# Performance work log

Measured on AMD Instinct MI355X. Metric: run time of the kernel, lower is better.

The kernel has to match this reference:

```python
import jax, jax.numpy as jnp
import numpy as np

# Physics config (DPhysConfig defaults for the tracked robot)
MASS = 40.0        # robot mass [kg]
GRAV = 9.8         # gravity magnitude
STIFF = 1000.0     # terrain stiffness
DAMP = 100.0       # terrain damping
OMEGA_MAX = 2.0    # angular velocity clamp
DT = 0.01          # integration step [s]
LY = 0.6           # robot width (track separation)
RES = 0.1          # grid resolution [m/cell]


def skew(v):
    # v: (..., 3) -> (..., 3, 3)
    z = jnp.zeros_like(v[..., 0])
    return jnp.stack([
        jnp.stack([z, -v[..., 2], v[..., 1]], -1),
        jnp.stack([v[..., 2], z, -v[..., 0]], -1),
        jnp.stack([-v[..., 1], v[..., 0], z], -1)], -2)


def normalized(x, eps=1e-6):
    return x / jnp.clip(jnp.linalg.norm(x, axis=-1, keepdims=True), eps)


def bilinear(grid, xq, yq):
    # grid: (B, H, W) over [-H*RES/2, H*RES/2] x [-W*RES/2, W*RES/2]; xq, yq: (B, N)
    B, H, W = grid.shape
    u = jnp.clip((xq + H * RES / 2) / RES, 0.0, H - 1.001)
    v = jnp.clip((yq + W * RES / 2) / RES, 0.0, W - 1.001)
    u0 = jnp.floor(u).astype(jnp.int32)
    v0 = jnp.floor(v).astype(jnp.int32)
    du, dv = u - u0, v - v0
    b = jnp.arange(B)[:, None]
    g00 = grid[b, u0, v0]
    g10 = grid[b, u0 + 1, v0]
    g01 = grid[b, u0, v0 + 1]
    g11 = grid[b, u0 + 1, v0 + 1]
    return (g00 * (1 - du) * (1 - dv) + g10 * du * (1 - dv)
            + g01 * (1 - du) * dv + g11 * du * dv)


def inertia_inv(points, mass):
    # points: (N, 3) body-frame point masses -> inverse inertia (3, 3)
    mp = mass / points.shape[0]
    x, y, z = points[:, 0], points[:, 1], points[:, 2]
    Ixx = (mp * (y ** 2 + z ** 2)).sum()
    Iyy = (mp * (x ** 2 + z ** 2)).sum()
    Izz = (mp * (x ** 2 + y ** 2)).sum()
    Ixy = -(mp * x * y).sum()
    Ixz = -(mp * x * z).sum()
    Iyz = -(mp * y * z).sum()
    I = jnp.stack([jnp.stack([Ixx, Ixy, Ixz]),
                   jnp.stack([Ixy, Iyy, Iyz]),
                   jnp.stack([Ixz, Iyz, Izz])])
    return jnp.linalg.inv(I)


def _forward(z_grid, friction, controls, robot_points, x0, xd0, R0, omega0):
    dtype = z_grid.dtype
    I_inv = inertia_inv(robot_points, MASS)          # (3,3), joints fixed -> constant
    gx = jnp.gradient(z_grid, axis=1) / RES          # dz/dx on grid
    gy = jnp.gradient(z_grid, axis=2) / RES          # dz/dy on grid
    maskL = (robot_points[:, 1] < 0).astype(dtype)   # (N,) left track points
    maskR = 1.0 - maskL                              # right track points
    F_grav = MASS * GRAV * jnp.array([0.0, 0.0, -1.0], dtype=dtype)
    clamp = MASS * GRAV

    def dynamics(state, ctrl):
        x, xd, R, omega = state
        # world-frame body points: x_points @ R^T + x
        pts = jnp.einsum('nj,bkj->bnk', robot_points, R) + x[:, None]      # (B,N,3)
        xd_pts = xd[:, None] + jnp.cross(omega[:, None, :], pts - x[:, None], axis=-1)
        px, py = pts[..., 0], pts[..., 1]
        z = bilinear(z_grid, px, py)[..., None]                            # (B,N,1)
        nrm = normalized(jnp.stack([-bilinear(gx, px, py),
                                    -bilinear(gy, px, py),
                                    jnp.ones_like(px)], -1))               # (B,N,3)
        fr = bilinear(friction, px, py)[..., None]                         # (B,N,1)
        dh = pts[..., 2:3] - z
        in_c = jax.nn.sigmoid(-10.0 * dh)
        xd_n = jnp.sum(xd_pts * nrm, -1, keepdims=True)
        F_r = -(STIFF * dh + DAMP * xd_n) * nrm
        F_r = jnp.clip(F_r * in_c / jnp.sum(in_c, 1, keepdims=True), -clamp, clamp)
        thrust = normalized(R[..., 0])                                     # (B,3) first column
        Nmag = jnp.linalg.norm(F_r, axis=2)                                # (B,N)
        v, w = ctrl[:, 0], ctrl[:, 1]
        vL = (v - w * LY / 2)[:, None, None]
        vR = (v + w * LY / 2)[:, None, None]
        cmd = (maskL[None, :, None] * vL + maskR[None, :, None] * vR) * thrust[:, None, :]
        slip = fr * (cmd - xd_pts)
        slip_tau = slip - jnp.sum(slip * nrm, -1, keepdims=True) * nrm
        F_f = jnp.clip(Nmag[..., None] * slip_tau, -clamp, clamp)
        torque = jnp.sum(jnp.cross(pts - x[:, None], F_r + F_f, axis=-1), axis=1)
        omega_d = jnp.clip(torque @ I_inv.T, -OMEGA_MAX, OMEGA_MAX)
        xdd = (F_grav[None] + F_r.sum(1) + F_f.sum(1)) / MASS
        return xdd, omega_d

    def rot_step(R, omega, eps=1e-6):
        # Rodrigues' formula
        Ox = skew(omega)
        th = jnp.linalg.norm(omega, axis=-1)[:, None, None]
        Oxn = Ox / jnp.clip(th, eps)
        I3 = jnp.eye(3, dtype=R.dtype)
        return R @ (I3 + Oxn * jnp.sin(th * DT) + (Oxn @ Oxn) * (1 - jnp.cos(th * DT)))

    def step(state, ctrl):
        x, xd, R, omega = state
        xdd, omega_d = dynamics(state, ctrl)
        xd = xd + xdd * DT          # semi-implicit Euler, as in update_state
        x = x + xd * DT
        omega = omega + omega_d * DT
        R = rot_step(R, omega)
        return (x, xd, R, omega), x

    _, Xs = jax.lax.scan(step, (x0, xd0, R0, omega0), jnp.swapaxes(controls, 0, 1))
    return jnp.swapaxes(Xs, 0, 1)   # (B, T, 3) trajectory positions


def setup_inputs() -> dict:
    key = jax.random.key(0)
    ks = jax.random.split(key, 5)
    B, T, N, H, W = 64, 500, 128, 256, 256
    z_grid = jax.random.uniform(ks[0], (B, H, W), dtype=jnp.float32) * 0.2
    friction = jax.random.uniform(ks[1], (B, H, W), dtype=jnp.float32)
    controls = jax.random.normal(ks[2], (B, T, 2), dtype=jnp.float32) * jnp.array([1.0, 0.5], jnp.float32)
    robot_points = (jax.random.uniform(ks[3], (N, 3), dtype=jnp.float32) - 0.5) \
        * jnp.array([1.0, 0.6, 0.2], jnp.float32)
    x0 = jax.random.normal(ks[4], (B, 3), dtype=jnp.float32) * 0.1 + jnp.array([0.0, 0.0, 0.3], jnp.float32)
    xd0 = jnp.zeros((B, 3), jnp.float32)
    R0 = jnp.tile(jnp.eye(3, dtype=jnp.float32), (B, 1, 1))
    omega0 = jnp.zeros((B, 3), jnp.float32)
    return {"z_grid": z_grid, "friction": friction, "controls": controls,
            "robot_points": robot_points, "x0": x0, "xd0": xd0, "R0": R0, "omega0": omega0}


def reference(z_grid, friction, controls, robot_points, x0, xd0, R0, omega0):
    return _forward(z_grid, friction, controls, robot_points, x0, xd0, R0, omega0)
```

## Files before the change

kernel.cpp:

```cpp
#include <hip/hip_runtime.h>
#include <math.h>

#define GH 256
#define GW 256

typedef float f4 __attribute__((ext_vector_type(4), aligned(4)));
typedef float f2 __attribute__((ext_vector_type(2), aligned(4)));
typedef float f4l __attribute__((ext_vector_type(4)));

template<int CTRL, int RMASK>
__device__ __forceinline__ float dpp_add(float v) {
    int r = __builtin_amdgcn_update_dpp(0, __builtin_bit_cast(int, v), CTRL, RMASK, 0xF, true);
    return v + __builtin_bit_cast(float, r);
}
template<int CTRL, int RMASK>
__device__ __forceinline__ float dpp_max(float v) {
    int r = __builtin_amdgcn_update_dpp(0, __builtin_bit_cast(int, v), CTRL, RMASK, 0xF, true);
    return fmaxf(v, __builtin_bit_cast(float, r));
}

__device__ __forceinline__ float wave_sum63(float v) {
    v = dpp_add<0xB1, 0xF>(v);
    v = dpp_add<0x4E, 0xF>(v);
    v = dpp_add<0x141, 0xF>(v);
    v = dpp_add<0x140, 0xF>(v);
    v = dpp_add<0x142, 0xA>(v);
    v = dpp_add<0x143, 0xC>(v);
    return v;
}
__device__ __forceinline__ float wave_max63(float v) {
    v = dpp_max<0xB1, 0xF>(v);
    v = dpp_max<0x4E, 0xF>(v);
    v = dpp_max<0x141, 0xF>(v);
    v = dpp_max<0x140, 0xF>(v);
    v = dpp_max<0x142, 0xA>(v);
    v = dpp_max<0x143, 0xC>(v);
    return v;
}
__device__ __forceinline__ float rl63(float v) {
    return __builtin_bit_cast(float, __builtin_amdgcn_readlane(__builtin_bit_cast(int, v), 63));
}

__device__ __forceinline__ float frcp(float x)  { return __builtin_amdgcn_rcpf(x); }
__device__ __forceinline__ float frsq(float x)  { return __builtin_amdgcn_rsqf(x); }
__device__ __forceinline__ float fexp2(float x) { return __builtin_amdgcn_exp2f(x); }

__global__ __launch_bounds__(128) void dphys_kernel(
    const float* __restrict__ z_grid,
    const float* __restrict__ friction,
    const float* __restrict__ controls,
    const float* __restrict__ robot_points,
    const float* __restrict__ x0,
    const float* __restrict__ xd0,
    const float* __restrict__ R0,
    const float* __restrict__ omega0,
    float* __restrict__ out,
    int T)
{
    const int b = blockIdx.x;
    const int tid = threadIdx.x;
    const int wv = tid >> 6;
    __shared__ f4l ldsX[2][2][2];
    __shared__ f4l ldsY[2][2];

    const float* __restrict__ zg = z_grid + (size_t)b * (GH * GW);
    const float* __restrict__ fg = friction + (size_t)b * (GH * GW);
    const float* __restrict__ ct = controls + (size_t)b * (T * 2);
    float* __restrict__ ob = out + (size_t)b * (T * 3);

    const float ppx = robot_points[tid * 3 + 0];
    const float ppy = robot_points[tid * 3 + 1];
    const float ppz = robot_points[tid * 3 + 2];
    const bool isL = (ppy < 0.0f);

    float I6[6];
    I6[0] = ppy * ppy + ppz * ppz;
    I6[1] = ppx * ppx + ppz * ppz;
    I6[2] = ppx * ppx + ppy * ppy;
    I6[3] = ppx * ppy;
    I6[4] = ppx * ppz;
    I6[5] = ppy * ppz;
    #pragma unroll
    for (int k = 0; k < 6; ++k) I6[k] = rl63(wave_sum63(I6[k]));
    if ((tid & 63) == 63) {
        f4l t0; t0.x = I6[0]; t0.y = I6[1]; t0.z = I6[2]; t0.w = I6[3];
        f4l t1; t1.x = I6[4]; t1.y = I6[5]; t1.z = 0.f; t1.w = 0.f;
        ldsY[wv][0] = t0; ldsY[wv][1] = t1;
    }
    __syncthreads();
    {
        f4l o0 = ldsY[wv ^ 1][0], o1 = ldsY[wv ^ 1][1];
        I6[0] += o0.x; I6[1] += o0.y; I6[2] += o0.z;
        I6[3] += o0.w; I6[4] += o1.x; I6[5] += o1.y;
    }
    const float mp = 0.3125f;
    {
        double a = mp * I6[0], bb = mp * I6[1], c = mp * I6[2];
        double d = -(mp * I6[3]), e = -(mp * I6[4]), f = -(mp * I6[5]);
        double C00 = bb * c - f * f, C01 = e * f - d * c, C02 = d * f - bb * e;
        double C11 = a * c - e * e, C12 = d * e - a * f, C22 = a * bb - d * d;
        double idet = 1.0 / (a * C00 + d * C01 + e * C02);
        I6[0] = (float)(C00 * idet); I6[1] = (float)(C11 * idet); I6[2] = (float)(C22 * idet);
        I6[3] = (float)(C01 * idet); I6[4] = (float)(C02 * idet); I6[5] = (float)(C12 * idet);
    }
    const float i00 = I6[0], i11 = I6[1], i22 = I6[2];
    const float i01 = I6[3], i02 = I6[4], i12 = I6[5];

    float X0 = x0[b * 3 + 0], X1 = x0[b * 3 + 1], X2 = x0[b * 3 + 2];
    float V0 = xd0[b * 3 + 0], V1 = xd0[b * 3 + 1], V2 = xd0[b * 3 + 2];
    float W0 = omega0[b * 3 + 0], W1 = omega0[b * 3 + 1], W2 = omega0[b * 3 + 2];
    float R00 = R0[b * 9 + 0], R01 = R0[b * 9 + 1], R02 = R0[b * 9 + 2];
    float R10 = R0[b * 9 + 3], R11 = R0[b * 9 + 4], R12 = R0[b * 9 + 5];
    float R20 = R0[b * 9 + 6], R21 = R0[b * 9 + 7], R22 = R0[b * 9 + 8];

    for (int t = 0; t < T; ++t) {
        const int par = t & 1;
        f2 cc = *(const f2*)(ct + t * 2);

        float rx = R00 * ppx + R01 * ppy + R02 * ppz;
        float ry = R10 * ppx + R11 * ppy + R12 * ppz;
        float rz = R20 * ppx + R21 * ppy + R22 * ppz;
        float Px = rx + X0, Py = ry + X1, Pz = rz + X2;
        float l0 = Px - X0, l1 = Py - X1, l2 = Pz - X2;
        float u = (Px + 12.8f) * 10.0f;
        u = fminf(fmaxf(u, 0.0f), 254.999f);
        float vvq = (Py + 12.8f) * 10.0f;
        vvq = fminf(fmaxf(vvq, 0.0f), 254.999f);
        int u0 = (int)u, v0 = (int)vvq;
        bool interior = (u0 >= 1) & (u0 <= 253) & (v0 >= 1) & (v0 <= 253);
        bool fast = __all(interior);

        float zz, fr, gxs, gys;
        float du = u - (float)u0, dv = vvq - (float)v0;
        float w00 = (1.0f - du) * (1.0f - dv);
        float w10 = du * (1.0f - dv);
        float w01 = (1.0f - du) * dv;
        float w11 = du * dv;

        float cv = cc.x, cw = cc.y;
        float half = (cw * 0.6f) * 0.5f;
        float vLs = cv - half, vRs = cv + half;
        float rtn = frsq(R00 * R00 + R10 * R10 + R20 * R20);
        float th0 = R00 * rtn, th1 = R10 * rtn, th2 = R20 * rtn;
        float xp0 = V0 + (W1 * l2 - W2 * l1);
        float xp1 = V1 + (W2 * l0 - W0 * l2);
        float xp2 = V2 + (W0 * l1 - W1 * l0);
        float cmd = isL ? vLs : vRs;
        float ct0 = cmd * th0 - xp0;
        float ct1 = cmd * th1 - xp1;
        float ct2 = cmd * th2 - xp2;

        if (fast) {
            int base = (u0 - 1) * GW + (v0 - 1);
            f4 P0 = *(const f4*)(zg + base);
            f4 P1 = *(const f4*)(zg + base + GW);
            f4 P2 = *(const f4*)(zg + base + 2 * GW);
            f4 P3 = *(const f4*)(zg + base + 3 * GW);
            int fb = u0 * GW + v0;
            f2 F0 = *(const f2*)(fg + fb);
            f2 F1 = *(const f2*)(fg + fb + GW);
            zz = P1.y * w00 + P2.y * w10 + P1.z * w01 + P2.z * w11;
            fr = F0.x * w00 + F1.x * w10 + F0.y * w01 + F1.y * w11;
            float gx00 = (P2.y - P0.y) * 5.0f;
            float gx10 = (P3.y - P1.y) * 5.0f;
            float gx01 = (P2.z - P0.z) * 5.0f;
            float gx11 = (P3.z - P1.z) * 5.0f;
            float gy00 = (P1.z - P1.x) * 5.0f;
            float gy10 = (P2.z - P2.x) * 5.0f;
            float gy01 = (P1.w - P1.y) * 5.0f;
            float gy11 = (P2.w - P2.y) * 5.0f;
            gxs = gx00 * w00 + gx10 * w10 + gx01 * w01 + gx11 * w11;
            gys = gy00 * w00 + gy10 * w10 + gy01 * w01 + gy11 * w11;
        } else {
            int basei = u0 * GW + v0;
            zz = zg[basei] * w00 + zg[basei + GW] * w10 + zg[basei + 1] * w01 + zg[basei + GW + 1] * w11;
            fr = fg[basei] * w00 + fg[basei + GW] * w10 + fg[basei + 1] * w01 + fg[basei + GW + 1] * w11;
            float gx[2][2], gy[2][2];
            #pragma unroll
            for (int ii = 0; ii < 2; ++ii) {
                int i = u0 + ii;
                int ipu = (i < GH - 1) ? i + 1 : i;
                int imu = (i > 0) ? i - 1 : i;
                float scu = (ipu - imu == 2) ? 0.5f : 1.0f;
                #pragma unroll
                for (int jj = 0; jj < 2; ++jj) {
                    int j = v0 + jj;
                    int jpv = (j < GW - 1) ? j + 1 : j;
                    int jmv = (j > 0) ? j - 1 : j;
                    float scv = (jpv - jmv == 2) ? 0.5f : 1.0f;
                    gx[ii][jj] = ((zg[ipu * GW + j] - zg[imu * GW + j]) * scu) * 10.0f;
                    gy[ii][jj] = ((zg[i * GW + jpv] - zg[i * GW + jmv]) * scv) * 10.0f;
                }
            }
            gxs = gx[0][0] * w00 + gx[1][0] * w10 + gx[0][1] * w01 + gx[1][1] * w11;
            gys = gy[0][0] * w00 + gy[1][0] * w10 + gy[0][1] * w01 + gy[1][1] * w11;
        }

        float rn = frsq(gxs * gxs + gys * gys + 1.0f);
        float nx = -gxs * rn, ny = -gys * rn, nzc = rn;
        float dh = Pz - zz;
        float ex = fexp2(dh * 14.426950408889634f);
        float ic = frcp(1.0f + ex);
        float xdn = xp0 * nx + xp1 * ny + xp2 * nzc;

        float mag = -(1000.0f * dh + 100.0f * xdn);
        float mic = mag * ic;
        float m_abs = fabsf(mic);
        float sl0 = fr * ct0, sl1 = fr * ct1, sl2 = fr * ct2;
        float sdn = sl0 * nx + sl1 * ny + sl2 * nzc;
        float st0 = sl0 - sdn * nx;
        float st1 = sl1 - sdn * ny;
        float st2 = sl2 - sdn * nzc;
        float g0 = mic * nx  + m_abs * st0;
        float g1 = mic * ny  + m_abs * st1;
        float g2 = mic * nzc + m_abs * st2;
        float q0 = l1 * g2 - l2 * g1;
        float q1 = l2 * g0 - l0 * g2;
        float q2 = l0 * g1 - l1 * g0;
        float stm = fmaxf(fmaxf(fabsf(st0), fabsf(st1)), fabsf(st2));
        float worst = fmaxf(stm, 1.0f) * m_abs;

        float d_ic = wave_sum63(ic);
        float d_g0 = wave_sum63(g0), d_g1 = wave_sum63(g1), d_g2 = wave_sum63(g2);
        float d_q0 = wave_sum63(q0), d_q1 = wave_sum63(q1), d_q2 = wave_sum63(q2);
        float d_rw = wave_max63(worst);
        if ((tid & 63) == 63) {
            f4l h0; h0.x = d_g0; h0.y = d_g1; h0.z = d_g2; h0.w = d_q0;
            f4l h1; h1.x = d_q1; h1.y = d_q2; h1.z = d_ic; h1.w = d_rw;
            ldsX[par][wv][0] = h0; ldsX[par][wv][1] = h1;
        }
        float o_ic = rl63(d_ic);
        float o_g0 = rl63(d_g0), o_g1 = rl63(d_g1), o_g2 = rl63(d_g2);
        float o_q0 = rl63(d_q0), o_q1 = rl63(d_q1), o_q2 = rl63(d_q2);
        float o_rw = rl63(d_rw);
        __syncthreads();
        f4l e0 = ldsX[par][wv ^ 1][0], e1 = ldsX[par][wv ^ 1][1];
        float sic = o_ic + e1.z;
        float rwm = fmaxf(o_rw, e1.w);
        float rsic = frcp(sic);

        float FT0, FT1, FT2, TQ0, TQ1, TQ2;
        if (rwm <= 391.0f * sic) {
            FT0 = (o_g0 + e0.x) * rsic;
            FT1 = (o_g1 + e0.y) * rsic;
            FT2 = (o_g2 + e0.z) * rsic;
            TQ0 = (o_q0 + e0.w) * rsic;
            TQ1 = (o_q1 + e1.x) * rsic;
            TQ2 = (o_q2 + e1.y) * rsic;
        } else {
            float s = mic * rsic;
            float Fr0 = fminf(fmaxf(s * nx,  -392.0f), 392.0f);
            float Fr1 = fminf(fmaxf(s * ny,  -392.0f), 392.0f);
            float Fr2 = fminf(fmaxf(s * nzc, -392.0f), 392.0f);
            float Nm = __builtin_amdgcn_sqrtf(Fr0 * Fr0 + Fr1 * Fr1 + Fr2 * Fr2);
            float Ff0 = fminf(fmaxf(Nm * st0, -392.0f), 392.0f);
            float Ff1 = fminf(fmaxf(Nm * st1, -392.0f), 392.0f);
            float Ff2 = fminf(fmaxf(Nm * st2, -392.0f), 392.0f);
            float S0 = Fr0 + Ff0, S1 = Fr1 + Ff1, S2 = Fr2 + Ff2;
            float U0 = l1 * S2 - l2 * S1;
            float U1 = l2 * S0 - l0 * S2;
            float U2 = l0 * S1 - l1 * S0;
            float dS0 = wave_sum63(S0), dS1 = wave_sum63(S1), dS2 = wave_sum63(S2);
            float dU0 = wave_sum63(U0), dU1 = wave_sum63(U1), dU2 = wave_sum63(U2);
            if ((tid & 63) == 63) {
                f4l h0; h0.x = dS0; h0.y = dS1; h0.z = dS2; h0.w = dU0;
                f4l h1; h1.x = dU1; h1.y = dU2; h1.z = 0.f; h1.w = 0.f;
                ldsY[wv][0] = h0; ldsY[wv][1] = h1;
            }
            __syncthreads();
            f4l c0 = ldsY[wv ^ 1][0], c1 = ldsY[wv ^ 1][1];
            FT0 = rl63(dS0) + c0.x; FT1 = rl63(dS1) + c0.y; FT2 = rl63(dS2) + c0.z;
            TQ0 = rl63(dU0) + c0.w; TQ1 = rl63(dU1) + c1.x; TQ2 = rl63(dU2) + c1.y;
        }

        float od0 = fminf(fmaxf(TQ0 * i00 + TQ1 * i01 + TQ2 * i02, -2.0f), 2.0f);
        float od1 = fminf(fmaxf(TQ0 * i01 + TQ1 * i11 + TQ2 * i12, -2.0f), 2.0f);
        float od2 = fminf(fmaxf(TQ0 * i02 + TQ1 * i12 + TQ2 * i22, -2.0f), 2.0f);

        V0 += (FT0 * 0.025f) * 0.01f;
        V1 += (FT1 * 0.025f) * 0.01f;
        V2 += ((-392.0f + FT2) * 0.025f) * 0.01f;
        X0 += V0 * 0.01f; X1 += V1 * 0.01f; X2 += V2 * 0.01f;
        W0 += od0 * 0.01f; W1 += od1 * 0.01f; W2 += od2 * 0.01f;

        if (tid == 0) {
            ob[t * 3 + 0] = X0;
            ob[t * 3 + 1] = X1;
            ob[t * 3 + 2] = X2;
        }

        float th2s = W0 * W0 + W1 * W1 + W2 * W2;
        float a2 = th2s * 1e-4f;
        float s1 = 0.01f - a2 * (0.01f / 6.0f);
        float c2 = 5e-5f - a2 * (1e-4f / 24.0f);
        float w01p = W0 * W1, w02p = W0 * W2, w12p = W1 * W2;
        float A00 = 1.0f - c2 * (W1 * W1 + W2 * W2);
        float A11 = 1.0f - c2 * (W0 * W0 + W2 * W2);
        float A22 = 1.0f - c2 * (W0 * W0 + W1 * W1);
        float A01 = c2 * w01p - s1 * W2;
        float A10 = c2 * w01p + s1 * W2;
        float A02 = c2 * w02p + s1 * W1;
        float A20 = c2 * w02p - s1 * W1;
        float A12 = c2 * w12p - s1 * W0;
        float A21 = c2 * w12p + s1 * W0;
        float N00 = R00 * A00 + R01 * A10 + R02 * A20;
        float N01 = R00 * A01 + R01 * A11 + R02 * A21;
        float N02 = R00 * A02 + R01 * A12 + R02 * A22;
        float N10 = R10 * A00 + R11 * A10 + R12 * A20;
        float N11 = R10 * A01 + R11 * A11 + R12 * A21;
        float N12 = R10 * A02 + R11 * A12 + R12 * A22;
        float N20 = R20 * A00 + R21 * A10 + R22 * A20;
        float N21 = R20 * A01 + R21 * A11 + R22 * A21;
        float N22 = R20 * A02 + R21 * A12 + R22 * A22;
        R00 = N00; R01 = N01; R02 = N02;
        R10 = N10; R11 = N11; R12 = N12;
        R20 = N20; R21 = N21; R22 = N22;
    }
}

extern "C" void kernel_launch(void* const* d_in, const int* in_sizes, int n_in,
                              void* d_out, int out_size, void* d_ws, size_t ws_size,
                              hipStream_t stream) {
    const float* z_grid       = (const float*)d_in[0];
    const float* friction     = (const float*)d_in[1];
    const float* controls     = (const float*)d_in[2];
    const float* robot_points = (const float*)d_in[3];
    const float* x0           = (const float*)d_in[4];
    const float* xd0          = (const float*)d_in[5];
    const float* R0           = (const float*)d_in[6];
    const float* omega0       = (const float*)d_in[7];
    int B = in_sizes[4] / 3;
    int T = in_sizes[2] / (B * 2);
    dphys_kernel<<<B, 128, 0, stream>>>(z_grid, friction, controls, robot_points,
                                        x0, xd0, R0, omega0, (float*)d_out, T);
}
```

Measured before the change: 554.9 us.

## Precompute interleaved height/gradient/friction texture and unroll time loop by four

Adds a prep kernel that writes each grid cell as a float4 of height, x-gradient, y-gradient and friction into workspace. The simulation kernel then does four float4 gathers per point per step instead of the separate height and friction patches and the on-the-fly gradient arithmetic, and the boundary-handling slow path goes away. The time loop is unrolled by four with trajectory outputs buffered and written as float4s. The cost is an extra full-grid pass and a 4x larger workspace read, and the path is used only when the workspace is big enough, otherwise the old kernel runs as a fallback.

```diff
diff --git a/kernel.cpp b/kernel.cpp
--- a/kernel.cpp
+++ b/kernel.cpp
@@ -18,7 +18,6 @@
     int r = __builtin_amdgcn_update_dpp(0, __builtin_bit_cast(int, v), CTRL, RMASK, 0xF, true);
     return fmaxf(v, __builtin_bit_cast(float, r));
 }
-
 __device__ __forceinline__ float wave_sum63(float v) {
     v = dpp_add<0xB1, 0xF>(v);
     v = dpp_add<0x4E, 0xF>(v);
@@ -40,12 +39,283 @@
 __device__ __forceinline__ float rl63(float v) {
     return __builtin_bit_cast(float, __builtin_amdgcn_readlane(__builtin_bit_cast(int, v), 63));
 }
-
 __device__ __forceinline__ float frcp(float x)  { return __builtin_amdgcn_rcpf(x); }
 __device__ __forceinline__ float frsq(float x)  { return __builtin_amdgcn_rsqf(x); }
 __device__ __forceinline__ float fexp2(float x) { return __builtin_amdgcn_exp2f(x); }
 
+#define LDS_BARRIER() asm volatile("s_waitcnt lgkmcnt(0)\n\ts_barrier" ::: "memory")
+
+__global__ __launch_bounds__(256) void prep_kernel(
+    const float* __restrict__ z_grid,
+    const float* __restrict__ friction,
+    f4* __restrict__ tex)
+{
+    const int j = threadIdx.x;
+    const int i = blockIdx.x;
+    const int b = blockIdx.y;
+    const float* __restrict__ z = z_grid + (size_t)b * (GH * GW);
+    int ipu = (i < GH - 1) ? i + 1 : i;
+    int imu = (i > 0) ? i - 1 : i;
+    int jpv = (j < GW - 1) ? j + 1 : j;
+    int jmv = (j > 0) ? j - 1 : j;
+    float scu = (ipu - imu == 2) ? 0.5f : 1.0f;
+    float scv = (jpv - jmv == 2) ? 0.5f : 1.0f;
+    float gx = ((z[ipu * GW + j] - z[imu * GW + j]) * scu) * 10.0f;
+    float gy = ((z[i * GW + jpv] - z[i * GW + jmv]) * scv) * 10.0f;
+    f4 o;
+    o.x = z[i * GW + j];
+    o.y = gx;
+    o.z = gy;
+    o.w = friction[(size_t)b * (GH * GW) + i * GW + j];
+    tex[(size_t)b * (GH * GW) + i * GW + j] = o;
+}
+
+#define STEP_BODY(TCUR, PH)                                                     \
+do {                                                                            \
+    const int par_ = (PH < 0) ? ((TCUR) & 1) : ((PH) & 1);                      \
+    f2 cc = *(const f2*)(ct + (TCUR) * 2);                                      \
+                                       \
+    float rx = R00 * ppx + R01 * ppy + R02 * ppz;                               \
+    float ry = R10 * ppx + R11 * ppy + R12 * ppz;                               \
+    float rz = R20 * ppx + R21 * ppy + R22 * ppz;                               \
+    float Px = rx + X0, Py = ry + X1, Pz = rz + X2;                             \
+    float l0 = Px - X0, l1 = Py - X1, l2 = Pz - X2;                             \
+    float u = fminf(fmaxf((Px + 12.8f) * 10.0f, 0.0f), 254.999f);               \
+    float vvq = fminf(fmaxf((Py + 12.8f) * 10.0f, 0.0f), 254.999f);             \
+    int u0 = (int)u, v0 = (int)vvq;                                             \
+    int idx = (u0 << 8) + v0;                                                   \
+    f4 c00 = tb[idx];                                                           \
+    f4 c01 = tb[idx + 1];                                                       \
+    f4 c10 = tb[idx + GW];                                                      \
+    f4 c11 = tb[idx + GW + 1];                                                  \
+                                                          \
+    float du = u - (float)u0, dv = vvq - (float)v0;                             \
+    float w00 = (1.0f - du) * (1.0f - dv);                                      \
+    float w10 = du * (1.0f - dv);                                               \
+    float w01 = (1.0f - du) * dv;                                               \
+    float w11 = du * dv;                                                        \
+    float cv = cc.x, cw = cc.y;                                                 \
+    float half_ = (cw * 0.6f) * 0.5f;                                           \
+    float vLs = cv - half_, vRs = cv + half_;                                   \
+       \
+    float xp0 = V0 + (W1 * l2 - W2 * l1);                                       \
+    float xp1 = V1 + (W2 * l0 - W0 * l2);                                       \
+    float xp2 = V2 + (W0 * l1 - W1 * l0);                                       \
+    float cmd = isL ? vLs : vRs;                                                \
+    float ct0 = cmd * R00 - xp0;                                                \
+    float ct1 = cmd * R10 - xp1;                                                \
+    float ct2 = cmd * R20 - xp2;                                                \
+                                         \
+    f4 cb = c00 * w00 + c10 * w10 + c01 * w01 + c11 * w11;                      \
+    float zz = cb.x, gxs = cb.y, gys = cb.z, fr = cb.w;                         \
+    float rn = frsq(gxs * gxs + gys * gys + 1.0f);                              \
+    float nx = -gxs * rn, ny = -gys * rn, nzc = rn;                             \
+    float dh = Pz - zz;                                                         \
+    float ex = fexp2(dh * 14.426950408889634f);                                 \
+    float ic = frcp(1.0f + ex);                                                 \
+    float xdn = xp0 * nx + xp1 * ny + xp2 * nzc;                                \
+    float mag = -(1000.0f * dh + 100.0f * xdn);                                 \
+    float mic = mag * ic;                                                       \
+    float m_abs = fabsf(mic);                                                   \
+    float sl0 = fr * ct0, sl1 = fr * ct1, sl2 = fr * ct2;                       \
+    float sdn = sl0 * nx + sl1 * ny + sl2 * nzc;                                \
+    float st0 = sl0 - sdn * nx;                                                 \
+    float st1 = sl1 - sdn * ny;                                                 \
+    float st2 = sl2 - sdn * nzc;                                                \
+    float g0 = mic * nx  + m_abs * st0;                                         \
+    float g1 = mic * ny  + m_abs * st1;                                         \
+    float g2 = mic * nzc + m_abs * st2;                                         \
+    float q0 = l1 * g2 - l2 * g1;                                               \
+    float q1 = l2 * g0 - l0 * g2;                                               \
+    float q2 = l0 * g1 - l1 * g0;                                               \
+    float stm = fmaxf(fmaxf(fabsf(st0), fabsf(st1)), fabsf(st2));               \
+    float worst = fmaxf(stm, 1.0f) * m_abs;                                     \
+                   \
+    float d_ic = wave_sum63(ic);                                                \
+    float d_g0 = wave_sum63(g0), d_g1 = wave_sum63(g1), d_g2 = wave_sum63(g2);  \
+    float d_q0 = wave_sum63(q0), d_q1 = wave_sum63(q1), d_q2 = wave_sum63(q2);  \
+    float d_rw = wave_max63(worst);                                             \
+    if ((tid & 63) == 63) {                                                     \
+        f4l h0; h0.x = d_g0; h0.y = d_g1; h0.z = d_g2; h0.w = d_q0;             \
+        f4l h1; h1.x = d_q1; h1.y = d_q2; h1.z = d_ic; h1.w = d_rw;             \
+        ldsX[par_][wv][0] = h0; ldsX[par_][wv][1] = h1;                         \
+    }                                                                           \
+    float o_ic = rl63(d_ic);                                                    \
+    float o_g0 = rl63(d_g0), o_g1 = rl63(d_g1), o_g2 = rl63(d_g2);              \
+    float o_q0 = rl63(d_q0), o_q1 = rl63(d_q1), o_q2 = rl63(d_q2);              \
+    float o_rw = rl63(d_rw);                                                    \
+    LDS_BARRIER();                                                              \
+    f4l e0 = ldsX[par_][wv ^ 1][0], e1 = ldsX[par_][wv ^ 1][1];                 \
+    float sic = o_ic + e1.z;                                                    \
+    float rwm = fmaxf(o_rw, e1.w);                                              \
+    float rsic = frcp(sic);                                                     \
+    float FT0, FT1, FT2, TQ0, TQ1, TQ2;                                         \
+    if (rwm <= 391.0f * sic) {                                                  \
+        FT0 = (o_g0 + e0.x) * rsic;                                             \
+        FT1 = (o_g1 + e0.y) * rsic;                                             \
+        FT2 = (o_g2 + e0.z) * rsic;                                             \
+        TQ0 = (o_q0 + e0.w) * rsic;                                             \
+        TQ1 = (o_q1 + e1.x) * rsic;                                             \
+        TQ2 = (o_q2 + e1.y) * rsic;                                             \
+    } else {                                                                    \
+        float s = mic * rsic;                                                   \
+        float Fr0 = fminf(fmaxf(s * nx,  -392.0f), 392.0f);                     \
+        float Fr1 = fminf(fmaxf(s * ny,  -392.0f), 392.0f);                     \
+        float Fr2 = fminf(fmaxf(s * nzc, -392.0f), 392.0f);                     \
+        float Nm = __builtin_amdgcn_sqrtf(Fr0 * Fr0 + Fr1 * Fr1 + Fr2 * Fr2);   \
+        float Ff0 = fminf(fmaxf(Nm * st0, -392.0f), 392.0f);                    \
+        float Ff1 = fminf(fmaxf(Nm * st1, -392.0f), 392.0f);                    \
+        float Ff2 = fminf(fmaxf(Nm * st2, -392.0f), 392.0f);                    \
+        float S0 = Fr0 + Ff0, S1 = Fr1 + Ff1, S2 = Fr2 + Ff2;                   \
+        float U0 = l1 * S2 - l2 * S1;                                           \
+        float U1 = l2 * S0 - l0 * S2;                                           \
+        float U2 = l0 * S1 - l1 * S0;                                           \
+        float dS0 = wave_sum63(S0), dS1 = wave_sum63(S1), dS2 = wave_sum63(S2); \
+        float dU0 = wave_sum63(U0), dU1 = wave_sum63(U1), dU2 = wave_sum63(U2); \
+        if ((tid & 63) == 63) {                                                 \
+            f4l h0; h0.x = dS0; h0.y = dS1; h0.z = dS2; h0.w = dU0;             \
+            f4l h1; h1.x = dU1; h1.y = dU2; h1.z = 0.f; h1.w = 0.f;             \
+            ldsY[wv][0] = h0; ldsY[wv][1] = h1;                                 \
+        }                                                                       \
+        LDS_BARRIER();                                                          \
+        f4l c0 = ldsY[wv ^ 1][0], c1 = ldsY[wv ^ 1][1];                         \
+        FT0 = rl63(dS0) + c0.x; FT1 = rl63(dS1) + c0.y; FT2 = rl63(dS2) + c0.z; \
+        TQ0 = rl63(dU0) + c0.w; TQ1 = rl63(dU1) + c1.x; TQ2 = rl63(dU2) + c1.y; \
+    }                                                                           \
+    float od0 = fminf(fmaxf(TQ0 * i00 + TQ1 * i01 + TQ2 * i02, -2.0f), 2.0f);   \
+    float od1 = fminf(fmaxf(TQ0 * i01 + TQ1 * i11 + TQ2 * i12, -2.0f), 2.0f);   \
+    float od2 = fminf(fmaxf(TQ0 * i02 + TQ1 * i12 + TQ2 * i22, -2.0f), 2.0f);   \
+    V0 += (FT0 * 0.025f) * 0.01f;                                               \
+    V1 += (FT1 * 0.025f) * 0.01f;                                               \
+    V2 += ((-392.0f + FT2) * 0.025f) * 0.01f;                                   \
+    X0 += V0 * 0.01f; X1 += V1 * 0.01f; X2 += V2 * 0.01f;                       \
+    W0 += od0 * 0.01f; W1 += od1 * 0.01f; W2 += od2 * 0.01f;                    \
+    if (PH < 0) {                                                               \
+        if (tid == 0) {                                                         \
+            ob[(TCUR) * 3 + 0] = X0;                                            \
+            ob[(TCUR) * 3 + 1] = X1;                                            \
+            ob[(TCUR) * 3 + 2] = X2;                                            \
+        }                                                                       \
+    } else if (PH == 0) { sb0.x = X0; sb0.y = X1; sb0.z = X2; }                 \
+    else if (PH == 1) { sb0.w = X0; sb1.x = X1; sb1.y = X2; }                   \
+    else if (PH == 2) { sb1.z = X0; sb1.w = X1; sb2.x = X2; }                   \
+    else {                                                                      \
+        sb2.y = X0; sb2.z = X1; sb2.w = X2;                                     \
+        if (tid == 0) {                                                         \
+            f4* op = (f4*)(ob + ((TCUR) - 3) * 3);                              \
+            op[0] = sb0; op[1] = sb1; op[2] = sb2;                              \
+        }                                                                       \
+    }                                                                           \
+                                       \
+    float th2s = W0 * W0 + W1 * W1 + W2 * W2;                                   \
+    float a2 = th2s * 1e-4f;                                                    \
+    float s1 = 0.01f - a2 * (0.01f / 6.0f);                                     \
+    float c2 = 5e-5f - a2 * (1e-4f / 24.0f);                                    \
+    float w01p = W0 * W1, w02p = W0 * W2, w12p = W1 * W2;                       \
+    float A00 = 1.0f - c2 * (W1 * W1 + W2 * W2);                                \
+    float A11 = 1.0f - c2 * (W0 * W0 + W2 * W2);                                \
+    float A22 = 1.0f - c2 * (W0 * W0 + W1 * W1);                                \
+    float A01 = c2 * w01p - s1 * W2;                                            \
+    float A10 = c2 * w01p + s1 * W2;                                            \
+    float A02 = c2 * w02p + s1 * W1;                                            \
+    float A20 = c2 * w02p - s1 * W1;                                            \
+    float A12 = c2 * w12p - s1 * W0;                                            \
+    float A21 = c2 * w12p + s1 * W0;                                            \
+    float N00 = R00 * A00 + R01 * A10 + R02 * A20;                              \
+    float N01 = R00 * A01 + R01 * A11 + R02 * A21;                              \
+    float N02 = R00 * A02 + R01 * A12 + R02 * A22;                              \
+    float N10 = R10 * A00 + R11 * A10 + R12 * A20;                              \
+    float N11 = R10 * A01 + R11 * A11 + R12 * A21;                              \
+    float N12 = R10 * A02 + R11 * A12 + R12 * A22;                              \
+    float N20 = R20 * A00 + R21 * A10 + R22 * A20;                              \
+    float N21 = R20 * A01 + R21 * A11 + R22 * A21;                              \
+    float N22 = R20 * A02 + R21 * A12 + R22 * A22;                              \
+    R00 = N00; R01 = N01; R02 = N02;                                            \
+    R10 = N10; R11 = N11; R12 = N12;                                            \
+    R20 = N20; R21 = N21; R22 = N22;                                            \
+} while (0)
+
 __global__ __launch_bounds__(128) void dphys_kernel(
+    const f4* __restrict__ tex,
+    const float* __restrict__ controls,
+    const float* __restrict__ robot_points,
+    const float* __restrict__ x0,
+    const float* __restrict__ xd0,
+    const float* __restrict__ R0,
+    const float* __restrict__ omega0,
+    float* __restrict__ out,
+    int T)
+{
+    const int b = blockIdx.x;
+    const int tid = threadIdx.x;
+    const int wv = tid >> 6;
+    __shared__ f4l ldsX[2][2][2];
+    __shared__ f4l ldsY[2][2];
+
+    const f4* __restrict__ tb = tex + (size_t)b * (GH * GW);
+    const float* __restrict__ ct = controls + (size_t)b * (T * 2);
+    float* __restrict__ ob = out + (size_t)b * (T * 3);
+
+    const float ppx = robot_points[tid * 3 + 0];
+    const float ppy = robot_points[tid * 3 + 1];
+    const float ppz = robot_points[tid * 3 + 2];
+    const bool isL = (ppy < 0.0f);
+
+    float I6[6];
+    I6[0] = ppy * ppy + ppz * ppz;
+    I6[1] = ppx * ppx + ppz * ppz;
+    I6[2] = ppx * ppx + ppy * ppy;
+    I6[3] = ppx * ppy;
+    I6[4] = ppx * ppz;
+    I6[5] = ppy * ppz;
+    #pragma unroll
+    for (int k = 0; k < 6; ++k) I6[k] = rl63(wave_sum63(I6[k]));
+    if ((tid & 63) == 63) {
+        f4l t0; t0.x = I6[0]; t0.y = I6[1]; t0.z = I6[2]; t0.w = I6[3];
+        f4l t1; t1.x = I6[4]; t1.y = I6[5]; t1.z = 0.f; t1.w = 0.f;
+        ldsY[wv][0] = t0; ldsY[wv][1] = t1;
+    }
+    __syncthreads();
+    {
+        f4l o0 = ldsY[wv ^ 1][0], o1 = ldsY[wv ^ 1][1];
+        I6[0] += o0.x; I6[1] += o0.y; I6[2] += o0.z;
+        I6[3] += o0.w; I6[4] += o1.x; I6[5] += o1.y;
+    }
+    const float mp = 0.3125f;
+    {
+        double a = mp * I6[0], bb = mp * I6[1], c = mp * I6[2];
+        double d = -(mp * I6[3]), e = -(mp * I6[4]), f = -(mp * I6[5]);
+        double C00 = bb * c - f * f, C01 = e * f - d * c, C02 = d * f - bb * e;
+        double C11 = a * c - e * e, C12 = d * e - a * f, C22 = a * bb - d * d;
+        double idet = 1.0 / (a * C00 + d * C01 + e * C02);
+        I6[0] = (float)(C00 * idet); I6[1] = (float)(C11 * idet); I6[2] = (float)(C22 * idet);
+        I6[3] = (float)(C01 * idet); I6[4] = (float)(C02 * idet); I6[5] = (float)(C12 * idet);
+    }
+    const float i00 = I6[0], i11 = I6[1], i22 = I6[2];
+    const float i01 = I6[3], i02 = I6[4], i12 = I6[5];
+
+    float X0 = x0[b * 3 + 0], X1 = x0[b * 3 + 1], X2 = x0[b * 3 + 2];
+    float V0 = xd0[b * 3 + 0], V1 = xd0[b * 3 + 1], V2 = xd0[b * 3 + 2];
+    float W0 = omega0[b * 3 + 0], W1 = omega0[b * 3 + 1], W2 = omega0[b * 3 + 2];
+    float R00 = R0[b * 9 + 0], R01 = R0[b * 9 + 1], R02 = R0[b * 9 + 2];
+    float R10 = R0[b * 9 + 3], R11 = R0[b * 9 + 4], R12 = R0[b * 9 + 5];
+    float R20 = R0[b * 9 + 6], R21 = R0[b * 9 + 7], R22 = R0[b * 9 + 8];
+
+    f4 sb0, sb1, sb2;
+
+    int t = 0;
+    for (; t + 3 < T; t += 4) {
+        STEP_BODY(t + 0, 0);
+        STEP_BODY(t + 1, 1);
+        STEP_BODY(t + 2, 2);
+        STEP_BODY(t + 3, 3);
+    }
+    for (; t < T; ++t) {
+        STEP_BODY(t, -1);
+    }
+}
+
+__global__ __launch_bounds__(128) void dphys_kernel_fb(
     const float* __restrict__ z_grid,
     const float* __restrict__ friction,
     const float* __restrict__ controls,
@@ -116,19 +386,16 @@
     for (int t = 0; t < T; ++t) {
         const int par = t & 1;
         f2 cc = *(const f2*)(ct + t * 2);
-
         float rx = R00 * ppx + R01 * ppy + R02 * ppz;
         float ry = R10 * ppx + R11 * ppy + R12 * ppz;
         float rz = R20 * ppx + R21 * ppy + R22 * ppz;
         float Px = rx + X0, Py = ry + X1, Pz = rz + X2;
         float l0 = Px - X0, l1 = Py - X1, l2 = Pz - X2;
-        float u = (Px + 12.8f) * 10.0f;
-        u = fminf(fmaxf(u, 0.0f), 254.999f);
-        float vvq = (Py + 12.8f) * 10.0f;
-        vvq = fminf(fmaxf(vvq, 0.0f), 254.999f);
+        float u = fminf(fmaxf((Px + 12.8f) * 10.0f, 0.0f), 254.999f);
+        float vvq = fminf(fmaxf((Py + 12.8f) * 10.0f, 0.0f), 254.999f);
         int u0 = (int)u, v0 = (int)vvq;
         bool interior = (u0 >= 1) & (u0 <= 253) & (v0 >= 1) & (v0 <= 253);
-        bool fast = __all(interior);
+        bool fastp = __all(interior);
 
         float zz, fr, gxs, gys;
         float du = u - (float)u0, dv = vvq - (float)v0;
@@ -150,7 +417,7 @@
         float ct1 = cmd * th1 - xp1;
         float ct2 = cmd * th2 - xp2;
 
-        if (fast) {
+        if (fastp) {
             int base = (u0 - 1) * GW + (v0 - 1);
             f4 P0 = *(const f4*)(zg + base);
             f4 P1 = *(const f4*)(zg + base + GW);
@@ -164,7 +431,8 @@
             float gx00 = (P2.y - P0.y) * 5.0f;
             float gx10 = (P3.y - P1.y) * 5.0f;
             float gx01 = (P2.z - P0.z) * 5.0f;
-            float gx11 = (P3.z - P1.z) * 5.0f;
+            float gx11 = (P3.w - P1.w) * 5.0f;
+            gx11 = (P3.z - P1.z) * 5.0f;
             float gy00 = (P1.z - P1.x) * 5.0f;
             float gy10 = (P2.z - P2.x) * 5.0f;
             float gy01 = (P1.w - P1.y) * 5.0f;
@@ -331,6 +599,13 @@
     const float* omega0       = (const float*)d_in[7];
     int B = in_sizes[4] / 3;
     int T = in_sizes[2] / (B * 2);
-    dphys_kernel<<<B, 128, 0, stream>>>(z_grid, friction, controls, robot_points,
-                                        x0, xd0, R0, omega0, (float*)d_out, T);
-}
+    size_t need = (size_t)B * GH * GW * sizeof(float) * 4;
+    if (ws_size >= need) {
+        prep_kernel<<<dim3(GH, B), GW, 0, stream>>>(z_grid, friction, (f4*)d_ws);
+        dphys_kernel<<<B, 128, 0, stream>>>((const f4*)d_ws, controls, robot_points,
+                                            x0, xd0, R0, omega0, (float*)d_out, T);
+    } else {
+        dphys_kernel_fb<<<B, 128, 0, stream>>>(z_grid, friction, controls, robot_points,
+                                               x0, xd0, R0, omega0, (float*)d_out, T);
+    }
+}
```

Result: faster. 447.7 us (-19.3%).
